# Kernel optimization log

Hardware: AMD Instinct MI355X
Metric: run time of the kernel (lower is better)

Reference implementation:

```python
import jax, jax.numpy as jnp
import numpy as np

N_EMBD = 2048
HIDDEN = 2 * N_EMBD        # 4096
ADAPT = HIDDEN // 16       # 256
B, S = 4, 2048


def _layernorm(x, g, b, eps=1e-5):
    mu = jnp.mean(x, axis=-1, keepdims=True)
    var = jnp.var(x, axis=-1, keepdims=True)
    return (x - mu) * jax.lax.rsqrt(var + eps) * g + b


def setup_inputs() -> dict:
    key = jax.random.key(0)
    ks = jax.random.split(key, 7)
    scale = 1.0 / np.sqrt(N_EMBD)
    adapt_scale = scale * 0.01
    return {
        "x": jax.random.normal(ks[0], (B, S, N_EMBD), dtype=jnp.float32),
        "W_up": jax.random.normal(ks[1], (HIDDEN, N_EMBD), dtype=jnp.float32) * scale,
        "W_gate": jax.random.normal(ks[2], (HIDDEN, N_EMBD), dtype=jnp.float32) * scale,
        "W_down": jax.random.normal(ks[3], (N_EMBD, HIDDEN), dtype=jnp.float32) * scale,
        "W_pre": jax.random.normal(ks[4], (ADAPT, N_EMBD), dtype=jnp.float32) * adapt_scale,
        "W_post": jax.random.normal(ks[5], (ADAPT, HIDDEN), dtype=jnp.float32) * adapt_scale,
        "W_proj": jax.random.normal(ks[6], (HIDDEN, ADAPT), dtype=jnp.float32) * adapt_scale,
        "ln_g": jnp.ones((ADAPT,), dtype=jnp.float32),
        "ln_b": jnp.zeros((ADAPT,), dtype=jnp.float32),
    }


def reference(x, W_up, W_gate, W_down, W_pre, W_post, W_proj, ln_g, ln_b):
    # SwiGLU trunk
    up = jnp.einsum('bsd,hd->bsh', x, W_up)
    gate = jnp.einsum('bsd,hd->bsh', x, W_gate)
    hidden = jax.nn.silu(gate) * up                      # [B,S,H]
    # Low-rank quadratic adapter
    adapt_in = _layernorm(jnp.einsum('bsd,ad->bsa', x, W_pre), ln_g, ln_b)       # [B,S,A]
    adapt_out = _layernorm(jnp.einsum('bsh,ah->bsa', hidden, W_post), ln_g, ln_b)  # [B,S,A]
    aw = jnp.einsum('bsa,bta->bst', adapt_in, adapt_out)  # [B,S,S]
    aw = jax.nn.silu(jnp.clip(aw, -5.0, 5.0))
    adapt = jnp.einsum('bst,bta->bsa', aw, adapt_in)      # [B,S,A]
    adapt = 0.1 * jnp.einsum('bsa,ha->bsh', adapt, W_proj)
    hidden = hidden + adapt
    out = jnp.einsum('bsh,dh->bsd', hidden, W_down)       # dropout p=0 -> identity
    return out
```

## Files before the change

### kernel.cpp

```cpp
#include <hip/hip_runtime.h>
#include <cstdint>
#include <cstddef>

typedef unsigned short u16;
typedef short short8 __attribute__((ext_vector_type(8)));
typedef float f32x4 __attribute__((ext_vector_type(4)));

__device__ __forceinline__ u16 f2bf(float f) {
  union { float f; unsigned u; } x; x.f = f;
  unsigned r = x.u + 0x7FFFu + ((x.u >> 16) & 1u);
  return (u16)(r >> 16);
}
__device__ __forceinline__ float b2f(u16 h) {
  union { unsigned u; float f; } x; x.u = ((unsigned)h) << 16;
  return x.f;
}
__device__ __forceinline__ float silu_f(float v) {
  return v / (1.f + __expf(-v));
}
__device__ __forceinline__ void gll(const u16* g, u16* l) {
  __builtin_amdgcn_global_load_lds((const __attribute__((address_space(1))) unsigned*)g,
                                   (__attribute__((address_space(3))) unsigned*)l, 16, 0, 0);
}

__global__ __launch_bounds__(256) void cvt7_k(const float4* __restrict__ s0,
                                              const float4* __restrict__ s1,
                                              const float4* __restrict__ s2,
                                              const float4* __restrict__ s3,
                                              const float4* __restrict__ s4,
                                              const float4* __restrict__ s5,
                                              const float4* __restrict__ s6,
                                              ushort4* __restrict__ dst) {
  const int i = blockIdx.x * 256 + threadIdx.x;
  const int o1 = 4194304, o2 = 6291456, o3 = 8388608, o4 = 10485760,
            o5 = 10616832, o6 = 10878976, o7 = 11141120;
  if (i >= o7) return;
  const float4* src;
  int base;
  if      (i < o1) { src = s0; base = 0;  }
  else if (i < o2) { src = s1; base = o1; }
  else if (i < o3) { src = s2; base = o2; }
  else if (i < o4) { src = s3; base = o3; }
  else if (i < o5) { src = s4; base = o4; }
  else if (i < o6) { src = s5; base = o5; }
  else             { src = s6; base = o6; }
  float4 v = src[i - base];
  ushort4 o;
  o.x = f2bf(v.x); o.y = f2bf(v.y); o.z = f2bf(v.z); o.w = f2bf(v.w);
  dst[i] = o;
}

__global__ __launch_bounds__(256) void red_ln_k(const float* __restrict__ part,
                                                const float* __restrict__ g,
                                                const float* __restrict__ b,
                                                u16* __restrict__ out,
                                                u16* __restrict__ outT, int Mtot) {
  const int row = blockIdx.x;
  const int a = threadIdx.x;
  const size_t stride = (size_t)Mtot * 256;
  const size_t base = (size_t)row * 256 + a;
  float v = part[base] + part[base + stride] + part[base + 2 * stride] + part[base + 3 * stride];
  float s = v, s2 = v * v;
#pragma unroll
  for (int o = 32; o; o >>= 1) { s += __shfl_down(s, o, 64); s2 += __shfl_down(s2, o, 64); }
  __shared__ float red[8];
  int l = a & 63, w = a >> 6;
  if (l == 0) { red[w] = s; red[4 + w] = s2; }
  __syncthreads();
  s  = red[0] + red[1] + red[2] + red[3];
  s2 = red[4] + red[5] + red[6] + red[7];
  float mu  = s * 0.00390625f;
  float var = s2 * 0.00390625f - mu * mu;
  float rs  = rsqrtf(var + 1e-5f);
  float o   = (v - mu) * rs * g[a] + b[a];
  u16 ob = f2bf(o);
  out[base] = ob;
  if (outT) {
    int bi = row >> 11, t = row & 2047;
    outT[((size_t)bi * 256 + a) * 2048 + t] = ob;
  }
}

__global__ __launch_bounds__(256) void red_k(const float* __restrict__ part,
                                             u16* __restrict__ out, int Mtot) {
  const int row = blockIdx.x;
  const int a = threadIdx.x;
  const size_t stride = (size_t)Mtot * 256;
  const size_t base = (size_t)row * 256 + a;
  float v = part[base] + part[base + stride] + part[base + 2 * stride] + part[base + 3 * stride];
  out[base] = f2bf(v);
}

template <int EPI>
__global__ __launch_bounds__(256) void gemm_bt(const u16* __restrict__ A,
                                               const u16* __restrict__ B,
                                               void* __restrict__ Cv,
                                               int M, int N, int K,
                                               long bA, long bB, long bC) {
  __shared__ u16 Al[128 * 64];
  __shared__ u16 Bl[128 * 64];
  const int tid  = threadIdx.x;
  const int bz   = blockIdx.z;
  const int brow = blockIdx.y * 128;
  const int bcol = blockIdx.x * 128;
  A += (size_t)bz * bA;
  B += (size_t)bz * bB;
  const int lane = tid & 63;
  const int w = tid >> 6, wr = w >> 1, wc = w & 1;
  const int srow = tid >> 3;
  const int scol = (tid & 7) * 8;

  f32x4 acc[4][4] = {};

  for (int kt = 0; kt < K; kt += 64) {
#pragma unroll
    for (int i = 0; i < 4; ++i)
      gll(A + (size_t)(brow + i * 32 + srow) * K + kt + scol, &Al[(i * 256 + tid) * 8]);
#pragma unroll
    for (int i = 0; i < 4; ++i)
      gll(B + (size_t)(bcol + i * 32 + srow) * K + kt + scol, &Bl[(i * 256 + tid) * 8]);
    __syncthreads();
#pragma unroll
    for (int kk = 0; kk < 2; ++kk) {
      short8 af[4], bfr[4];
      const int ko = kk * 32 + (lane >> 4) * 8;
#pragma unroll
      for (int m = 0; m < 4; ++m)
        af[m] = *(const short8*)&Al[(wr * 64 + m * 16 + (lane & 15)) * 64 + ko];
#pragma unroll
      for (int n = 0; n < 4; ++n)
        bfr[n] = *(const short8*)&Bl[(wc * 64 + n * 16 + (lane & 15)) * 64 + ko];
#pragma unroll
      for (int m = 0; m < 4; ++m)
#pragma unroll
        for (int n = 0; n < 4; ++n)
          acc[m][n] = __builtin_amdgcn_mfma_f32_16x16x32_bf16(af[m], bfr[n], acc[m][n], 0, 0, 0);
    }
    __syncthreads();
  }

  const int col0 = bcol + wc * 64 + (lane & 15);
  const int row0 = brow + wr * 64 + ((lane >> 4) << 2);
  u16* Cb = (u16*)Cv + (size_t)bz * bC;
#pragma unroll
  for (int m = 0; m < 4; ++m)
#pragma unroll
    for (int j = 0; j < 4; ++j) {
      size_t roff = (size_t)(row0 + m * 16 + j) * N + col0;
#pragma unroll
      for (int n = 0; n < 4; ++n) {
        float v = acc[m][n][j];
        if (EPI == 2) {
          v = fminf(5.f, fmaxf(-5.f, v));
          v = silu_f(v);
        }
        Cb[roff + n * 16] = f2bf(v);
      }
    }
}

__global__ __launch_bounds__(256) void gemm_sk(const u16* __restrict__ A,
                                               const u16* __restrict__ B,
                                               float* __restrict__ part,
                                               int M, int N, int Kfull, int Kc,
                                               long bA, long bB, int Mtot) {
  const int z  = blockIdx.z;
  const int b  = z >> 2, sk = z & 3;
  const int brow = blockIdx.y * 128;
  const int bcol = blockIdx.x * 128;
  A += (size_t)b * bA + (size_t)sk * Kc;
  B += (size_t)b * bB + (size_t)sk * Kc;

  __shared__ u16 Al[128 * 64];
  __shared__ u16 Bl[128 * 64];
  const int tid  = threadIdx.x;
  const int lane = tid & 63;
  const int w = tid >> 6, wr = w >> 1, wc = w & 1;
  const int srow = tid >> 3;
  const int scol = (tid & 7) * 8;

  f32x4 acc[4][4] = {};

  for (int kt = 0; kt < Kc; kt += 64) {
#pragma unroll
    for (int i = 0; i < 4; ++i)
      gll(A + (size_t)(brow + i * 32 + srow) * Kfull + kt + scol, &Al[(i * 256 + tid) * 8]);
#pragma unroll
    for (int i = 0; i < 4; ++i)
      gll(B + (size_t)(bcol + i * 32 + srow) * Kfull + kt + scol, &Bl[(i * 256 + tid) * 8]);
    __syncthreads();
#pragma unroll
    for (int kk = 0; kk < 2; ++kk) {
      short8 af[4], bfr[4];
      const int ko = kk * 32 + (lane >> 4) * 8;
#pragma unroll
      for (int m = 0; m < 4; ++m)
        af[m] = *(const short8*)&Al[(wr * 64 + m * 16 + (lane & 15)) * 64 + ko];
#pragma unroll
      for (int n = 0; n < 4; ++n)
        bfr[n] = *(const short8*)&Bl[(wc * 64 + n * 16 + (lane & 15)) * 64 + ko];
#pragma unroll
      for (int m = 0; m < 4; ++m)
#pragma unroll
        for (int n = 0; n < 4; ++n)
          acc[m][n] = __builtin_amdgcn_mfma_f32_16x16x32_bf16(af[m], bfr[n], acc[m][n], 0, 0, 0);
    }
    __syncthreads();
  }

  const int col0 = bcol + wc * 64 + (lane & 15);
  const int row0 = brow + wr * 64 + ((lane >> 4) << 2);
  float* P = part + ((size_t)sk * Mtot + (size_t)b * M) * N;
#pragma unroll
  for (int m = 0; m < 4; ++m)
#pragma unroll
    for (int j = 0; j < 4; ++j) {
      size_t roff = (size_t)(row0 + m * 16 + j) * N + col0;
#pragma unroll
      for (int n = 0; n < 4; ++n) P[roff + n * 16] = acc[m][n][j];
    }
}

template <int EPI>
__global__ __launch_bounds__(512, 2) void gemm256(const u16* __restrict__ A,
                                                  const u16* __restrict__ B,
                                                  void* __restrict__ Cv,
                                                  const u16* __restrict__ H,
                                                  int M, int N, int K,
                                                  long bA, long bB, long bC) {
  __shared__ __align__(16) u16 As[32768];
  __shared__ __align__(16) u16 Bs[32768];

  const int tid = threadIdx.x;
  const int bz  = blockIdx.z;
  A += (size_t)bz * bA;
  B += (size_t)bz * bB;

  const int gx = gridDim.x;
  const int nwg = gx * gridDim.y;
  int orig = blockIdx.y * gx + blockIdx.x;
  {
    int q = nwg >> 3, r = nwg & 7;
    int xcd = orig & 7, idx = orig >> 3;
    orig = (xcd < r) ? xcd * (q + 1) + idx : r * (q + 1) + (xcd - r) * q + idx;
  }
  const int brow = (orig / gx) * 256;
  const int bcol = (orig % gx) * 256;

  const int lane = tid & 63;
  const int wid  = tid >> 6;
  const int wm = wid >> 2, wn = wid & 3;

  const int srow = tid >> 3;
  const int scol = ((((tid & 7) << 4) ^ ((srow & 7) << 4)) >> 1);
  const u16* Abase = A + (size_t)(brow + srow) * K + scol;
  const u16* Bbase = B + (size_t)(bcol + srow) * K + scol;

  const int fr  = lane & 15;
  const int cs0 = ((((lane >> 4) << 4) ^ ((lane & 7) << 4)) >> 1);
  const int cs1 = cs0 ^ 32;
  const int bro = (wn & 1) * 64;

  const int NT = K >> 6;
  f32x4 acc[8][4] = {};

  auto stageAll = [&](int tt) {
    const int ktn = tt << 6;
    const int bb = (tt & 1) * 2;
#pragma unroll
    for (int h = 0; h < 2; ++h) {
      const u16* s = Abase + (size_t)(h * 128) * K + ktn;
      u16* d = &As[(bb + h) * 8192 + tid * 8];
      gll(s, d); gll(s + (size_t)64 * K, d + 4096);
    }
#pragma unroll
    for (int h = 0; h < 2; ++h) {
      const u16* s = Bbase + (size_t)(h * 128) * K + ktn;
      u16* d = &Bs[(bb + h) * 8192 + tid * 8];
      gll(s, d); gll(s + (size_t)64 * K, d + 4096);
    }
  };

#define RD_A(DST, BASE, ROFF, CS)                                           \
  {                                                                         \
    _Pragma("unroll")                                                       \
    for (int m = 0; m < 4; ++m)                                             \
      DST[m] = *(const short8*)(BASE + (ROFF + m * 16 + fr) * 64 + CS);     \
  }
#define RD_B(DST, BASE, CS)                                                 \
  {                                                                         \
    _Pragma("unroll")                                                       \
    for (int n = 0; n < 4; ++n)                                             \
      DST[n] = *(const short8*)(BASE + (bro + n * 16 + fr) * 64 + CS);      \
  }
#define MFMA16(AB, AR, BR)                                                  \
  __builtin_amdgcn_sched_barrier(0);                                        \
  __builtin_amdgcn_s_setprio(1);                                            \
  {                                                                         \
    _Pragma("unroll")                                                       \
    for (int m = 0; m < 4; ++m)                                             \
      _Pragma("unroll")                                                     \
      for (int n = 0; n < 4; ++n)                                           \
        acc[AB + m][n] = __builtin_amdgcn_mfma_f32_16x16x32_bf16(           \
            AR[m], BR[n], acc[AB + m][n], 0, 0, 0);                         \
  }                                                                         \
  __builtin_amdgcn_s_setprio(0);                                            \
  __builtin_amdgcn_sched_barrier(0);

  short8 aR0[4], aR1[4], bR0[4], bR1[4];

  stageAll(0);
  asm volatile("s_waitcnt vmcnt(0)" ::: "memory");
  __builtin_amdgcn_s_barrier();
  {
    const u16* aH = &As[wm * 8192];
    const u16* bH = &Bs[(wn >> 1) * 8192];
    RD_A(aR0, aH, 0, cs0)
    RD_B(bR0, bH, cs0)
  }

  for (int t = 0; t < NT; ++t) {
    const int cur = t & 1;
    const u16* aH  = &As[(cur * 2 + wm) * 8192];
    const u16* bH  = &Bs[(cur * 2 + (wn >> 1)) * 8192];
    const u16* aHn = &As[((cur ^ 1) * 2 + wm) * 8192];
    const u16* bHn = &Bs[((cur ^ 1) * 2 + (wn >> 1)) * 8192];
    const bool pf = (t + 1 < NT);

    if (pf) stageAll(t + 1);
    RD_A(aR1, aH, 64, cs0)
    MFMA16(0, aR0, bR0)

    RD_A(aR0, aH, 0, cs1)
    RD_B(bR1, bH, cs1)
    MFMA16(4, aR1, bR0)

    RD_A(aR1, aH, 64, cs1)
    MFMA16(0, aR0, bR1)
    asm volatile("s_waitcnt vmcnt(0)" ::: "memory");
    __builtin_amdgcn_s_barrier();

    if (pf) {
      RD_A(aR0, aHn, 0, cs0)
      RD_B(bR0, bHn, cs0)
    }
    MFMA16(4, aR1, bR1)
    __builtin_amdgcn_s_barrier();
  }
#undef RD_A
#undef RD_B
#undef MFMA16

  const int col0 = bcol + wn * 64 + fr;
  const int row0 = brow + wm * 128 + ((lane >> 4) << 2);

  if (EPI == 0) {
    float* Cf = (float*)Cv + (size_t)bz * bC;
#pragma unroll
    for (int m = 0; m < 8; ++m)
#pragma unroll
      for (int j = 0; j < 4; ++j) {
        size_t roff = (size_t)(row0 + m * 16 + j) * N + col0;
#pragma unroll
        for (int n = 0; n < 4; ++n) Cf[roff + n * 16] = acc[m][n][j];
      }
  } else if (EPI == 1) {
    u16* Cb = (u16*)Cv + (size_t)bz * bC;
#pragma unroll
    for (int m = 0; m < 8; ++m)
#pragma unroll
      for (int j = 0; j < 4; ++j) {
        size_t roff = (size_t)(row0 + m * 16 + j) * N + col0;
#pragma unroll
        for (int n = 0; n < 4; ++n) Cb[roff + n * 16] = f2bf(acc[m][n][j]);
      }
  } else if (EPI == 2) {
    u16* Cb = (u16*)Cv + (size_t)bz * bC;
#pragma unroll
    for (int m = 0; m < 8; ++m)
#pragma unroll
      for (int j = 0; j < 4; ++j) {
        size_t roff = (size_t)(row0 + m * 16 + j) * N + col0;
#pragma unroll
        for (int n = 0; n < 4; ++n) {
          float v = acc[m][n][j];
          v = fminf(5.f, fmaxf(-5.f, v));
          Cb[roff + n * 16] = f2bf(silu_f(v));
        }
      }
  } else if (EPI == 3) {
    u16* Cb = (u16*)Cv + (size_t)bz * bC;
    const u16* Hb = H + (size_t)bz * bC;
#pragma unroll
    for (int m = 0; m < 8; ++m)
#pragma unroll
      for (int j = 0; j < 4; ++j) {
        size_t roff = (size_t)(row0 + m * 16 + j) * N + col0;
#pragma unroll
        for (int n = 0; n < 4; ++n) {
          size_t idx = roff + n * 16;
          Cb[idx] = f2bf(b2f(Hb[idx]) + 0.1f * acc[m][n][j]);
        }
      }
  } else {
    u16* Cb = (u16*)Cv + (size_t)bz * bC;
    const u16* Hb = H + (size_t)bz * bC;
#pragma unroll
    for (int m = 0; m < 8; ++m)
#pragma unroll
      for (int j = 0; j < 4; ++j) {
        size_t roff = (size_t)(row0 + m * 16 + j) * N + col0;
#pragma unroll
        for (int n = 0; n < 4; ++n) {
          size_t idx = roff + n * 16;
          Cb[idx] = f2bf(silu_f(acc[m][n][j]) * b2f(Hb[idx]));
        }
      }
  }
}

extern "C" void kernel_launch(void* const* d_in, const int* in_sizes, int n_in,
                              void* d_out, int out_size, void* d_ws, size_t ws_size,
                              hipStream_t stream) {
  const float* x      = (const float*)d_in[0];
  const float* W_up   = (const float*)d_in[1];
  const float* W_gate = (const float*)d_in[2];
  const float* W_down = (const float*)d_in[3];
  const float* W_pre  = (const float*)d_in[4];
  const float* W_post = (const float*)d_in[5];
  const float* W_proj = (const float*)d_in[6];
  const float* ln_g   = (const float*)d_in[7];
  const float* ln_b   = (const float*)d_in[8];
  (void)in_sizes; (void)n_in; (void)out_size; (void)ws_size;

  const int D = 2048, Hh = 4096, A_ = 256, Bn = 4, S = 2048, M = 8192;

  char* p = (char*)d_ws;
  u16* xb      = (u16*)p; p += (size_t)M * D * 2;
  u16* Wup_b   = (u16*)p; p += (size_t)Hh * D * 2;
  u16* Wgate_b = (u16*)p; p += (size_t)Hh * D * 2;
  u16* Wdown_b = (u16*)p; p += (size_t)D * Hh * 2;
  u16* Wpre_b  = (u16*)p; p += (size_t)A_ * D * 2;
  u16* Wpost_b = (u16*)p; p += (size_t)A_ * Hh * 2;
  u16* Wproj_b = (u16*)p; p += (size_t)Hh * A_ * 2;
  u16* hidden  = (u16*)p; p += (size_t)M * Hh * 2;
  u16* scratch = (u16*)p; p += (size_t)M * Hh * 2;
  char* q = (char*)scratch;
  u16*   aw        = (u16*)q; q += (size_t)Bn * S * S * 2;
  u16*   adapt_in  = (u16*)q; q += (size_t)M * A_ * 2;
  u16*   adapt_inT = (u16*)q; q += (size_t)M * A_ * 2;
  u16*   adapt_out = (u16*)q; q += (size_t)M * A_ * 2;
  u16*   adaptb    = (u16*)q; q += (size_t)M * A_ * 2;
  float* part = (float*)Wup_b;

  cvt7_k<<<dim3(43520), dim3(256), 0, stream>>>((const float4*)x, (const float4*)W_up,
                                                (const float4*)W_gate, (const float4*)W_down,
                                                (const float4*)W_pre, (const float4*)W_post,
                                                (const float4*)W_proj, (ushort4*)xb);

  gemm256<1><<<dim3(Hh / 256, M / 256, 1), 512, 0, stream>>>(xb, Wup_b, hidden, nullptr,
                                                             M, Hh, D, 0, 0, 0);
  gemm256<4><<<dim3(Hh / 256, M / 256, 1), 512, 0, stream>>>(xb, Wgate_b, hidden, hidden,
                                                             M, Hh, D, 0, 0, 0);

  gemm_sk<<<dim3(A_ / 128, M / 128, 4), 256, 0, stream>>>(xb, Wpre_b, part,
                                                          M, A_, D, D / 4, 0, 0, M);
  red_ln_k<<<dim3(M), 256, 0, stream>>>(part, ln_g, ln_b, adapt_in, adapt_inT, M);

  gemm_sk<<<dim3(A_ / 128, M / 128, 4), 256, 0, stream>>>(hidden, Wpost_b, part,
                                                          M, A_, Hh, Hh / 4, 0, 0, M);
  red_ln_k<<<dim3(M), 256, 0, stream>>>(part, ln_g, ln_b, adapt_out, nullptr, M);

  gemm_bt<2><<<dim3(S / 128, S / 128, Bn), 256, 0, stream>>>(adapt_in, adapt_out, aw,
                                                             S, S, A_,
                                                             (long)S * A_, (long)S * A_, (long)S * S);

  gemm_sk<<<dim3(A_ / 128, S / 128, Bn * 4), 256, 0, stream>>>(aw, adapt_inT, part,
                                                               S, A_, S, S / 4,
                                                               (long)S * S, (long)A_ * S, M);
  red_k<<<dim3(M), 256, 0, stream>>>(part, adaptb, M);

  gemm256<3><<<dim3(Hh / 256, M / 256, 1), 512, 0, stream>>>(adaptb, Wproj_b, hidden, hidden,
                                                             M, Hh, A_, 0, 0, 0);

  gemm256<0><<<dim3(D / 256, M / 256, 1), 512, 0, stream>>>(hidden, Wdown_b, d_out, nullptr,
                                                            M, D, Hh, 0, 0, 0);
}
```

Baseline: 632.6 us.

## Fold adapter projection into down-proj via precomputed W_down·W_proj and new GEMM pipeline

Rather than adding 0.1*adapt@W_proj^T into hidden and then multiplying by W_down, the code precomputes Wdp = 0.1*W_down@W_proj (2048x256) and runs the final GEMM as hidden@W_down^T + adaptb@Wdp^T in one kernel with two K loops. This drops the separate M x 4096 x 256 GEMM and its read-modify-write of the bf16 hidden buffer. The gemm256 main loop is also rewritten into a four-phase schedule that prefetches two k-tiles ahead and uses a different warp-to-tile mapping. Wdp is rounded to bf16 and hidden is no longer rounded after the adapter add, so numerics change slightly.

```diff
diff --git a/kernel.cpp b/kernel.cpp
--- a/kernel.cpp
+++ b/kernel.cpp
@@ -22,6 +22,7 @@
   __builtin_amdgcn_global_load_lds((const __attribute__((address_space(1))) unsigned*)g,
                                    (__attribute__((address_space(3))) unsigned*)l, 16, 0, 0);
 }
+__device__ __forceinline__ short8 ld8(const u16* p) { return *(const short8*)p; }
 
 __global__ __launch_bounds__(256) void cvt7_k(const float4* __restrict__ s0,
                                               const float4* __restrict__ s1,
@@ -29,12 +30,11 @@
                                               const float4* __restrict__ s3,
                                               const float4* __restrict__ s4,
                                               const float4* __restrict__ s5,
-                                              const float4* __restrict__ s6,
                                               ushort4* __restrict__ dst) {
   const int i = blockIdx.x * 256 + threadIdx.x;
   const int o1 = 4194304, o2 = 6291456, o3 = 8388608, o4 = 10485760,
-            o5 = 10616832, o6 = 10878976, o7 = 11141120;
-  if (i >= o7) return;
+            o5 = 10616832, o6 = 10878976;
+  if (i >= o6) return;
   const float4* src;
   int base;
   if      (i < o1) { src = s0; base = 0;  }
@@ -42,12 +42,17 @@
   else if (i < o3) { src = s2; base = o2; }
   else if (i < o4) { src = s3; base = o3; }
   else if (i < o5) { src = s4; base = o4; }
-  else if (i < o6) { src = s5; base = o5; }
-  else             { src = s6; base = o6; }
+  else             { src = s5; base = o5; }
   float4 v = src[i - base];
   ushort4 o;
   o.x = f2bf(v.x); o.y = f2bf(v.y); o.z = f2bf(v.z); o.w = f2bf(v.w);
   dst[i] = o;
+}
+
+__global__ __launch_bounds__(256) void tcvt_k(const float* __restrict__ in,
+                                              u16* __restrict__ out) {
+  const int h = blockIdx.x, a = threadIdx.x;
+  out[(size_t)a * 4096 + h] = f2bf(in[(size_t)h * 256 + a]);
 }
 
 __global__ __launch_bounds__(256) void red_ln_k(const float* __restrict__ part,
@@ -82,13 +87,13 @@
 }
 
 __global__ __launch_bounds__(256) void red_k(const float* __restrict__ part,
-                                             u16* __restrict__ out, int Mtot) {
+                                             u16* __restrict__ out, int Mtot, float scale) {
   const int row = blockIdx.x;
   const int a = threadIdx.x;
   const size_t stride = (size_t)Mtot * 256;
   const size_t base = (size_t)row * 256 + a;
   float v = part[base] + part[base + stride] + part[base + 2 * stride] + part[base + 3 * stride];
-  out[base] = f2bf(v);
+  out[base] = f2bf(v * scale);
 }
 
 template <int EPI>
@@ -221,20 +226,133 @@
     }
 }
 
+__device__ __forceinline__ void pipe256(const u16* Abase, const u16* Bbase, int K,
+                                        u16* As, u16* Bs, int tid, int wm, int wn,
+                                        int lane, f32x4 (*acc)[4]) {
+  const int fr  = lane & 15;
+  const int cs0 = ((((lane >> 4) << 4) ^ ((lane & 7) << 4)) >> 1);
+  const int cs1 = cs0 ^ 32;
+  const int NT = K >> 6;
+
+  auto stage = [&](const u16* OPb, u16* L, int tt, int half) {
+    const u16* s = OPb + (size_t)(half * 128) * K + (tt << 6);
+    u16* d = &L[((tt & 1) * 2 + half) * 8192 + tid * 8];
+    gll(s, d); gll(s + (size_t)64 * K, d + 4096);
+  };
+
+  stage(Abase, As, 0, 0); stage(Bbase, Bs, 0, 0);
+  stage(Abase, As, 0, 1); stage(Bbase, Bs, 0, 1);
+  if (NT > 1) {
+    stage(Abase, As, 1, 0); stage(Bbase, Bs, 1, 0);
+    stage(Abase, As, 1, 1); stage(Bbase, Bs, 1, 1);
+    asm volatile("s_waitcnt vmcnt(8)" ::: "memory");
+  } else {
+    asm volatile("s_waitcnt vmcnt(0)" ::: "memory");
+  }
+  __builtin_amdgcn_s_barrier();
+
+  const int aoff0 = (wm * 64 + fr) * 64;
+  const int boff0 = (wn * 32 + fr) * 64;
+
+  short8 aLo[8], aHi[8], bb[4];
+
+  for (int t = 0; t < NT; ++t) {
+    const u16* h0a = &As[(t & 1) * 16384];
+    const u16* h0b = &Bs[(t & 1) * 16384];
+    const u16* h1a = h0a + 8192;
+    const u16* h1b = h0b + 8192;
+    const bool pf = (t + 2 < NT);
+
+#pragma unroll
+    for (int m = 0; m < 4; ++m) {
+      aLo[m * 2]     = ld8(h0a + aoff0 + m * 1024 + cs0);
+      aLo[m * 2 + 1] = ld8(h0a + aoff0 + m * 1024 + cs1);
+    }
+#pragma unroll
+    for (int n = 0; n < 2; ++n) {
+      bb[n * 2]     = ld8(h0b + boff0 + n * 1024 + cs0);
+      bb[n * 2 + 1] = ld8(h0b + boff0 + n * 1024 + cs1);
+    }
+    __builtin_amdgcn_s_barrier();
+    asm volatile("s_waitcnt lgkmcnt(0)" ::: "memory");
+    __builtin_amdgcn_s_setprio(1);
+#pragma unroll
+    for (int m = 0; m < 4; ++m)
+#pragma unroll
+      for (int n = 0; n < 2; ++n) {
+        acc[m][n] = __builtin_amdgcn_mfma_f32_16x16x32_bf16(aLo[m*2],   bb[n*2],   acc[m][n], 0, 0, 0);
+        acc[m][n] = __builtin_amdgcn_mfma_f32_16x16x32_bf16(aLo[m*2+1], bb[n*2+1], acc[m][n], 0, 0, 0);
+      }
+    __builtin_amdgcn_s_setprio(0);
+    __builtin_amdgcn_s_barrier();
+
+#pragma unroll
+    for (int m = 0; m < 4; ++m) {
+      aHi[m * 2]     = ld8(h1a + aoff0 + m * 1024 + cs0);
+      aHi[m * 2 + 1] = ld8(h1a + aoff0 + m * 1024 + cs1);
+    }
+    if (pf) { stage(Abase, As, t + 2, 0); stage(Bbase, Bs, t + 2, 0); }
+    __builtin_amdgcn_s_barrier();
+    asm volatile("s_waitcnt lgkmcnt(0)" ::: "memory");
+    __builtin_amdgcn_s_setprio(1);
+#pragma unroll
+    for (int m = 0; m < 4; ++m)
+#pragma unroll
+      for (int n = 0; n < 2; ++n) {
+        acc[4+m][n] = __builtin_amdgcn_mfma_f32_16x16x32_bf16(aHi[m*2],   bb[n*2],   acc[4+m][n], 0, 0, 0);
+        acc[4+m][n] = __builtin_amdgcn_mfma_f32_16x16x32_bf16(aHi[m*2+1], bb[n*2+1], acc[4+m][n], 0, 0, 0);
+      }
+    __builtin_amdgcn_s_setprio(0);
+    __builtin_amdgcn_s_barrier();
+
+#pragma unroll
+    for (int n = 0; n < 2; ++n) {
+      bb[n * 2]     = ld8(h1b + boff0 + n * 1024 + cs0);
+      bb[n * 2 + 1] = ld8(h1b + boff0 + n * 1024 + cs1);
+    }
+    if (pf) stage(Abase, As, t + 2, 1);
+    __builtin_amdgcn_s_barrier();
+    asm volatile("s_waitcnt lgkmcnt(0)" ::: "memory");
+    __builtin_amdgcn_s_setprio(1);
+#pragma unroll
+    for (int m = 0; m < 4; ++m)
+#pragma unroll
+      for (int n = 0; n < 2; ++n) {
+        acc[m][2+n] = __builtin_amdgcn_mfma_f32_16x16x32_bf16(aLo[m*2],   bb[n*2],   acc[m][2+n], 0, 0, 0);
+        acc[m][2+n] = __builtin_amdgcn_mfma_f32_16x16x32_bf16(aLo[m*2+1], bb[n*2+1], acc[m][2+n], 0, 0, 0);
+      }
+    __builtin_amdgcn_s_setprio(0);
+    __builtin_amdgcn_s_barrier();
+
+    if (pf) stage(Bbase, Bs, t + 2, 1);
+    __builtin_amdgcn_s_barrier();
+    asm volatile("s_waitcnt lgkmcnt(0)" ::: "memory");
+    __builtin_amdgcn_s_setprio(1);
+#pragma unroll
+    for (int m = 0; m < 4; ++m)
+#pragma unroll
+      for (int n = 0; n < 2; ++n) {
+        acc[4+m][2+n] = __builtin_amdgcn_mfma_f32_16x16x32_bf16(aHi[m*2],   bb[n*2],   acc[4+m][2+n], 0, 0, 0);
+        acc[4+m][2+n] = __builtin_amdgcn_mfma_f32_16x16x32_bf16(aHi[m*2+1], bb[n*2+1], acc[4+m][2+n], 0, 0, 0);
+      }
+    __builtin_amdgcn_s_setprio(0);
+    if (t + 2 < NT)      { asm volatile("s_waitcnt vmcnt(8)" ::: "memory"); }
+    else if (t + 1 < NT) { asm volatile("s_waitcnt vmcnt(0)" ::: "memory"); }
+    __builtin_amdgcn_s_barrier();
+  }
+}
+
 template <int EPI>
 __global__ __launch_bounds__(512, 2) void gemm256(const u16* __restrict__ A,
                                                   const u16* __restrict__ B,
                                                   void* __restrict__ Cv,
                                                   const u16* __restrict__ H,
-                                                  int M, int N, int K,
-                                                  long bA, long bB, long bC) {
+                                                  int N, int K,
+                                                  const u16* __restrict__ A2,
+                                                  const u16* __restrict__ B2, int K2) {
   __shared__ __align__(16) u16 As[32768];
   __shared__ __align__(16) u16 Bs[32768];
-
   const int tid = threadIdx.x;
-  const int bz  = blockIdx.z;
-  A += (size_t)bz * bA;
-  B += (size_t)bz * bB;
 
   const int gx = gridDim.x;
   const int nwg = gx * gridDim.y;
@@ -250,172 +368,37 @@
   const int lane = tid & 63;
   const int wid  = tid >> 6;
   const int wm = wid >> 2, wn = wid & 3;
-
   const int srow = tid >> 3;
   const int scol = ((((tid & 7) << 4) ^ ((srow & 7) << 4)) >> 1);
-  const u16* Abase = A + (size_t)(brow + srow) * K + scol;
-  const u16* Bbase = B + (size_t)(bcol + srow) * K + scol;
-
-  const int fr  = lane & 15;
-  const int cs0 = ((((lane >> 4) << 4) ^ ((lane & 7) << 4)) >> 1);
-  const int cs1 = cs0 ^ 32;
-  const int bro = (wn & 1) * 64;
-
-  const int NT = K >> 6;
+
   f32x4 acc[8][4] = {};
 
-  auto stageAll = [&](int tt) {
-    const int ktn = tt << 6;
-    const int bb = (tt & 1) * 2;
-#pragma unroll
-    for (int h = 0; h < 2; ++h) {
-      const u16* s = Abase + (size_t)(h * 128) * K + ktn;
-      u16* d = &As[(bb + h) * 8192 + tid * 8];
-      gll(s, d); gll(s + (size_t)64 * K, d + 4096);
-    }
-#pragma unroll
-    for (int h = 0; h < 2; ++h) {
-      const u16* s = Bbase + (size_t)(h * 128) * K + ktn;
-      u16* d = &Bs[(bb + h) * 8192 + tid * 8];
-      gll(s, d); gll(s + (size_t)64 * K, d + 4096);
-    }
-  };
-
-#define RD_A(DST, BASE, ROFF, CS)                                           \
-  {                                                                         \
-    _Pragma("unroll")                                                       \
-    for (int m = 0; m < 4; ++m)                                             \
-      DST[m] = *(const short8*)(BASE + (ROFF + m * 16 + fr) * 64 + CS);     \
-  }
-#define RD_B(DST, BASE, CS)                                                 \
-  {                                                                         \
-    _Pragma("unroll")                                                       \
-    for (int n = 0; n < 4; ++n)                                             \
-      DST[n] = *(const short8*)(BASE + (bro + n * 16 + fr) * 64 + CS);      \
-  }
-#define MFMA16(AB, AR, BR)                                                  \
-  __builtin_amdgcn_sched_barrier(0);                                        \
-  __builtin_amdgcn_s_setprio(1);                                            \
-  {                                                                         \
-    _Pragma("unroll")                                                       \
-    for (int m = 0; m < 4; ++m)                                             \
-      _Pragma("unroll")                                                     \
-      for (int n = 0; n < 4; ++n)                                           \
-        acc[AB + m][n] = __builtin_amdgcn_mfma_f32_16x16x32_bf16(           \
-            AR[m], BR[n], acc[AB + m][n], 0, 0, 0);                         \
-  }                                                                         \
-  __builtin_amdgcn_s_setprio(0);                                            \
-  __builtin_amdgcn_sched_barrier(0);
-
-  short8 aR0[4], aR1[4], bR0[4], bR1[4];
-
-  stageAll(0);
-  asm volatile("s_waitcnt vmcnt(0)" ::: "memory");
-  __builtin_amdgcn_s_barrier();
-  {
-    const u16* aH = &As[wm * 8192];
-    const u16* bH = &Bs[(wn >> 1) * 8192];
-    RD_A(aR0, aH, 0, cs0)
-    RD_B(bR0, bH, cs0)
-  }
-
-  for (int t = 0; t < NT; ++t) {
-    const int cur = t & 1;
-    const u16* aH  = &As[(cur * 2 + wm) * 8192];
-    const u16* bH  = &Bs[(cur * 2 + (wn >> 1)) * 8192];
-    const u16* aHn = &As[((cur ^ 1) * 2 + wm) * 8192];
-    const u16* bHn = &Bs[((cur ^ 1) * 2 + (wn >> 1)) * 8192];
-    const bool pf = (t + 1 < NT);
-
-    if (pf) stageAll(t + 1);
-    RD_A(aR1, aH, 64, cs0)
-    MFMA16(0, aR0, bR0)
-
-    RD_A(aR0, aH, 0, cs1)
-    RD_B(bR1, bH, cs1)
-    MFMA16(4, aR1, bR0)
-
-    RD_A(aR1, aH, 64, cs1)
-    MFMA16(0, aR0, bR1)
-    asm volatile("s_waitcnt vmcnt(0)" ::: "memory");
-    __builtin_amdgcn_s_barrier();
-
-    if (pf) {
-      RD_A(aR0, aHn, 0, cs0)
-      RD_B(bR0, bHn, cs0)
-    }
-    MFMA16(4, aR1, bR1)
-    __builtin_amdgcn_s_barrier();
-  }
-#undef RD_A
-#undef RD_B
-#undef MFMA16
-
-  const int col0 = bcol + wn * 64 + fr;
-  const int row0 = brow + wm * 128 + ((lane >> 4) << 2);
-
-  if (EPI == 0) {
-    float* Cf = (float*)Cv + (size_t)bz * bC;
-#pragma unroll
-    for (int m = 0; m < 8; ++m)
-#pragma unroll
-      for (int j = 0; j < 4; ++j) {
-        size_t roff = (size_t)(row0 + m * 16 + j) * N + col0;
-#pragma unroll
-        for (int n = 0; n < 4; ++n) Cf[roff + n * 16] = acc[m][n][j];
-      }
-  } else if (EPI == 1) {
-    u16* Cb = (u16*)Cv + (size_t)bz * bC;
-#pragma unroll
-    for (int m = 0; m < 8; ++m)
-#pragma unroll
-      for (int j = 0; j < 4; ++j) {
-        size_t roff = (size_t)(row0 + m * 16 + j) * N + col0;
-#pragma unroll
-        for (int n = 0; n < 4; ++n) Cb[roff + n * 16] = f2bf(acc[m][n][j]);
-      }
-  } else if (EPI == 2) {
-    u16* Cb = (u16*)Cv + (size_t)bz * bC;
-#pragma unroll
-    for (int m = 0; m < 8; ++m)
-#pragma unroll
-      for (int j = 0; j < 4; ++j) {
-        size_t roff = (size_t)(row0 + m * 16 + j) * N + col0;
-#pragma unroll
-        for (int n = 0; n < 4; ++n) {
-          float v = acc[m][n][j];
-          v = fminf(5.f, fmaxf(-5.f, v));
-          Cb[roff + n * 16] = f2bf(silu_f(v));
+  pipe256(A + (size_t)(brow + srow) * K + scol,
+          B + (size_t)(bcol + srow) * K + scol, K, As, Bs, tid, wm, wn, lane, acc);
+  if (K2 > 0)
+    pipe256(A2 + (size_t)(brow + srow) * K2 + scol,
+            B2 + (size_t)(bcol + srow) * K2 + scol, K2, As, Bs, tid, wm, wn, lane, acc);
+
+  const int fr = lane & 15;
+#pragma unroll
+  for (int m = 0; m < 8; ++m) {
+    const int mrow = (m < 4) ? (wm * 64 + m * 16) : (128 + wm * 64 + (m - 4) * 16);
+#pragma unroll
+    for (int j = 0; j < 4; ++j) {
+      const size_t roff = (size_t)(brow + mrow + ((lane >> 4) << 2) + j) * N + bcol + fr;
+#pragma unroll
+      for (int n = 0; n < 4; ++n) {
+        const int ncol = (n < 2) ? (wn * 32 + n * 16) : (128 + wn * 32 + (n - 2) * 16);
+        const size_t idx = roff + ncol;
+        if (EPI == 0) {
+          ((float*)Cv)[idx] = acc[m][n][j];
+        } else if (EPI == 1) {
+          ((u16*)Cv)[idx] = f2bf(acc[m][n][j]);
+        } else {
+          ((u16*)Cv)[idx] = f2bf(silu_f(acc[m][n][j]) * b2f(H[idx]));
         }
       }
-  } else if (EPI == 3) {
-    u16* Cb = (u16*)Cv + (size_t)bz * bC;
-    const u16* Hb = H + (size_t)bz * bC;
-#pragma unroll
-    for (int m = 0; m < 8; ++m)
-#pragma unroll
-      for (int j = 0; j < 4; ++j) {
-        size_t roff = (size_t)(row0 + m * 16 + j) * N + col0;
-#pragma unroll
-        for (int n = 0; n < 4; ++n) {
-          size_t idx = roff + n * 16;
-          Cb[idx] = f2bf(b2f(Hb[idx]) + 0.1f * acc[m][n][j]);
-        }
-      }
-  } else {
-    u16* Cb = (u16*)Cv + (size_t)bz * bC;
-    const u16* Hb = H + (size_t)bz * bC;
-#pragma unroll
-    for (int m = 0; m < 8; ++m)
-#pragma unroll
-      for (int j = 0; j < 4; ++j) {
-        size_t roff = (size_t)(row0 + m * 16 + j) * N + col0;
-#pragma unroll
-        for (int n = 0; n < 4; ++n) {
-          size_t idx = roff + n * 16;
-          Cb[idx] = f2bf(silu_f(acc[m][n][j]) * b2f(Hb[idx]));
-        }
-      }
+    }
   }
 }
 
@@ -442,7 +425,7 @@
   u16* Wdown_b = (u16*)p; p += (size_t)D * Hh * 2;
   u16* Wpre_b  = (u16*)p; p += (size_t)A_ * D * 2;
   u16* Wpost_b = (u16*)p; p += (size_t)A_ * Hh * 2;
-  u16* Wproj_b = (u16*)p; p += (size_t)Hh * A_ * 2;
+  u16* WprojT  = (u16*)p; p += (size_t)Hh * A_ * 2;
   u16* hidden  = (u16*)p; p += (size_t)M * Hh * 2;
   u16* scratch = (u16*)p; p += (size_t)M * Hh * 2;
   char* q = (char*)scratch;
@@ -451,17 +434,24 @@
   u16*   adapt_inT = (u16*)q; q += (size_t)M * A_ * 2;
   u16*   adapt_out = (u16*)q; q += (size_t)M * A_ * 2;
   u16*   adaptb    = (u16*)q; q += (size_t)M * A_ * 2;
+  float* wdp_part  = (float*)q; q += (size_t)4 * 2048 * 256 * 4;
+  u16*   Wdp_b     = (u16*)q; q += (size_t)2048 * 256 * 2;
   float* part = (float*)Wup_b;
 
-  cvt7_k<<<dim3(43520), dim3(256), 0, stream>>>((const float4*)x, (const float4*)W_up,
+  cvt7_k<<<dim3(42496), dim3(256), 0, stream>>>((const float4*)x, (const float4*)W_up,
                                                 (const float4*)W_gate, (const float4*)W_down,
                                                 (const float4*)W_pre, (const float4*)W_post,
-                                                (const float4*)W_proj, (ushort4*)xb);
-
-  gemm256<1><<<dim3(Hh / 256, M / 256, 1), 512, 0, stream>>>(xb, Wup_b, hidden, nullptr,
-                                                             M, Hh, D, 0, 0, 0);
-  gemm256<4><<<dim3(Hh / 256, M / 256, 1), 512, 0, stream>>>(xb, Wgate_b, hidden, hidden,
-                                                             M, Hh, D, 0, 0, 0);
+                                                (ushort4*)xb);
+  tcvt_k<<<dim3(4096), dim3(256), 0, stream>>>(W_proj, WprojT);
+
+  gemm_sk<<<dim3(A_ / 128, 2048 / 128, 4), 256, 0, stream>>>(Wdown_b, WprojT, wdp_part,
+                                                             2048, A_, Hh, Hh / 4, 0, 0, 2048);
+  red_k<<<dim3(2048), 256, 0, stream>>>(wdp_part, Wdp_b, 2048, 0.1f);
+
+  gemm256<1><<<dim3(Hh / 256, M / 256), 512, 0, stream>>>(xb, Wup_b, hidden, nullptr,
+                                                          Hh, D, nullptr, nullptr, 0);
+  gemm256<4><<<dim3(Hh / 256, M / 256), 512, 0, stream>>>(xb, Wgate_b, hidden, hidden,
+                                                          Hh, D, nullptr, nullptr, 0);
 
   gemm_sk<<<dim3(A_ / 128, M / 128, 4), 256, 0, stream>>>(xb, Wpre_b, part,
                                                           M, A_, D, D / 4, 0, 0, M);
@@ -478,11 +468,8 @@
   gemm_sk<<<dim3(A_ / 128, S / 128, Bn * 4), 256, 0, stream>>>(aw, adapt_inT, part,
                                                                S, A_, S, S / 4,
                                                                (long)S * S, (long)A_ * S, M);
-  red_k<<<dim3(M), 256, 0, stream>>>(part, adaptb, M);
-
-  gemm256<3><<<dim3(Hh / 256, M / 256, 1), 512, 0, stream>>>(adaptb, Wproj_b, hidden, hidden,
-                                                             M, Hh, A_, 0, 0, 0);
-
-  gemm256<0><<<dim3(D / 256, M / 256, 1), 512, 0, stream>>>(hidden, Wdown_b, d_out, nullptr,
-                                                            M, D, Hh, 0, 0, 0);
-}
+  red_k<<<dim3(M), 256, 0, stream>>>(part, adaptb, M, 1.0f);
+
+  gemm256<0><<<dim3(D / 256, M / 256), 512, 0, stream>>>(hidden, Wdown_b, d_out, nullptr,
+                                                         D, Hh, adaptb, Wdp_b, A_);
+}
```

Result: faster. 605.6 us (-4.3%).
